# Optimization experiments

Hardware: AMD Instinct MI355X
Metric: run time of the kernel (lower is better)

## Reference

```python
import jax, jax.numpy as jnp
import numpy as np
from jax import lax

EPS = 1e-05
DN = ('NHWC', 'HWIO', 'NHWC')


def setup_inputs() -> dict:
    key = jax.random.key(0)
    k1, k2, k3 = jax.random.split(key, 3)
    x = jax.random.normal(k1, (16, 64, 64, 128), dtype=jnp.float32)
    kernel = jax.random.normal(k2, (3, 3, 128, 256), dtype=jnp.float32) * 0.05
    bias = jax.random.normal(k3, (256,), dtype=jnp.float32) * 0.01
    alpha = jnp.ones((1,), dtype=jnp.float32)
    return {"x": x, "kernel": kernel, "bias": bias, "alpha": alpha}


def reference(x, kernel, bias, alpha):
    # dot-product conv: <patch, W> per output channel  -> [B,H,W,O]
    dot = lax.conv_general_dilated(x, kernel, (1, 1), 'SAME', dimension_numbers=DN)
    # per-patch squared norm ||x_patch||^2 via conv of x^2 with ones kernel -> [B,H,W,1]
    ones_k = jnp.ones(kernel.shape[:-1] + (1,), dtype=x.dtype)
    patch_sq = lax.conv_general_dilated(x * x, ones_k, (1, 1), 'SAME', dimension_numbers=DN)
    # per-output-channel squared kernel norm ||W_o||^2 -> [O]
    kernel_sq = jnp.sum(kernel * kernel, axis=(0, 1, 2))
    # ||x - W||^2 = ||x||^2 - 2<x,W> + ||W||^2
    dist_sq = patch_sq - 2.0 * dot + kernel_sq
    y = (dot * dot) / (dist_sq + EPS)
    y = y + bias
    out_features = kernel.shape[-1]
    scale = (jnp.sqrt(jnp.float32(out_features)) / jnp.log1p(jnp.float32(out_features))) ** alpha
    return y * scale
```

## Files before the change

### kernel.cpp

```cpp
#include <hip/hip_runtime.h>
#include <stdint.h>


#define HH 64
#define WW 64
#define CC 128
#define OO 256
#define HP 66
#define WP 66
#define NPIX (16 * HP * WP)
#define KTOT 1152
#define NKT 18
#define EPSV 1e-5f

#define BM 256
#define BN 128
#define SLOT_BYTES 49152
#define B_OFF 32768
#define SMEM_TOTAL (3 * SLOT_BYTES + 1024)

typedef short short8 __attribute__((ext_vector_type(8)));
typedef float f32x4 __attribute__((ext_vector_type(4)));

__device__ __forceinline__ unsigned short f2bf(float f) {
  unsigned u = __builtin_bit_cast(unsigned, f);
  u += 0x7fffu + ((u >> 16) & 1u);
  return (unsigned short)(u >> 16);
}

__device__ __forceinline__ void gload_lds16(const void* g, void* l) {
  __builtin_amdgcn_global_load_lds(
      (const __attribute__((address_space(1))) unsigned int*)g,
      (__attribute__((address_space(3))) unsigned int*)l,
      16, 0, 0);
}

#define FENCE() asm volatile("" ::: "memory")
#define BAR() do { FENCE(); __builtin_amdgcn_s_barrier(); FENCE(); } while (0)

__global__ __launch_bounds__(256) void prep_x(const float* __restrict__ x,
                                              unsigned short* __restrict__ xp,
                                              float* __restrict__ s2p) {
  int lane = threadIdx.x & 63;
  int wv = (blockIdx.x << 2) + (threadIdx.x >> 6);
  for (int gw = wv; gw < NPIX; gw += 4096) {
    int b = gw / (HP * WP);
    int rem = gw - b * (HP * WP);
    int hp = rem / WP;
    int wp = rem - hp * WP;
    float2 v = make_float2(0.f, 0.f);
    if (hp >= 1 && hp <= HH && wp >= 1 && wp <= WW) {
      const float2* src = (const float2*)(x + (size_t)(((b * HH) + hp - 1) * WW + (wp - 1)) * CC);
      v = src[lane];
    }
    ushort2 o2;
    o2.x = f2bf(v.x);
    o2.y = f2bf(v.y);
    ((ushort2*)(xp + (size_t)gw * CC))[lane] = o2;
    float ss = v.x * v.x + v.y * v.y;
    #pragma unroll
    for (int off = 32; off > 0; off >>= 1) ss += __shfl_down(ss, off);
    if (lane == 0) s2p[gw] = ss;
  }
}

__global__ __launch_bounds__(256) void prep_w(const float* __restrict__ kern,
                                              unsigned short* __restrict__ wt,
                                              float* __restrict__ ksq) {
  int o = blockIdx.x;
  int t = threadIdx.x;
  float acc = 0.f;
  for (int k = t; k < KTOT; k += 256) {
    float v = kern[(size_t)k * OO + o];
    wt[(size_t)o * KTOT + k] = f2bf(v);
    acc += v * v;
  }
  __shared__ float red[256];
  red[t] = acc;
  __syncthreads();
  #pragma unroll
  for (int s = 128; s > 0; s >>= 1) {
    if (t < s) red[t] += red[t + s];
    __syncthreads();
  }
  if (t == 0) ksq[o] = red[0];
}

__global__ __launch_bounds__(512, 2) void yat_main(
    const unsigned short* __restrict__ xp,
    const unsigned short* __restrict__ wt,
    const float* __restrict__ s2p,
    const float* __restrict__ ksq,
    const float* __restrict__ bias,
    const float* __restrict__ alpha,
    float* __restrict__ out) {
  extern __shared__ char smem[];

  int tid = threadIdx.x;
  int wid = tid >> 6, lane = tid & 63;

  int bid = blockIdx.x;
  int swz = ((bid & 7) << 6) + (bid >> 3);
  int mt = swz >> 1, nt = swz & 1;
  int m0 = mt << 8;
  int n0 = nt << 7;

  int cg = (((tid & 7) ^ ((tid >> 3) & 7)) << 3);
  const unsigned short* aSrc[4];
  #pragma unroll
  for (int q = 0; q < 4; ++q) {
    int r = (q << 6) + (tid >> 3);
    int p = m0 + r;
    int b = p >> 12, h = (p >> 6) & 63, w = p & 63;
    aSrc[q] = xp + (size_t)((b * HP + h) * WP + w) * CC + cg;
  }
  const unsigned short* bSrc[2];
  #pragma unroll
  for (int q = 0; q < 2; ++q) {
    int r = (q << 6) + (tid >> 3);
    bSrc[q] = wt + (size_t)(n0 + r) * KTOT + cg;
  }

  auto STAGE = [&](int t, int soff) {
    int tap = t >> 1;
    int dy = tap / 3;
    int dx = tap - dy * 3;
    int koff = (dy * WP + dx) * CC + ((t & 1) << 6);
    char* da = smem + soff + (wid << 10);
    #pragma unroll
    for (int q = 0; q < 4; ++q)
      gload_lds16(aSrc[q] + koff, da + (q << 13));
    int kb = t << 6;
    char* db = smem + soff + B_OFF + (wid << 10);
    #pragma unroll
    for (int q = 0; q < 2; ++q)
      gload_lds16(bSrc[q] + kb, db + (q << 13));
  };

  int wr = wid >> 1, wcn = wid & 1;
  int rA0 = (wr << 6) + (lane & 15);
  int rB0 = (wcn << 6) + (lane & 15);
  int xsw = lane & 7;
  int co0 = (((lane >> 4) ^ xsw) << 4);
  int co1 = ((((lane >> 4) + 4) ^ xsw) << 4);

  f32x4 acc[4][4] = {};

  STAGE(0, 0);
  STAGE(1, SLOT_BYTES);

  int soff = 0;
  int stoff = 2 * SLOT_BYTES;
  for (int i = 0; i < NKT; ++i) {
    if (i < NKT - 2) STAGE(i + 2, stoff);
    if (i < NKT - 2)      asm volatile("s_waitcnt vmcnt(12)" ::: "memory");
    else if (i == NKT - 2) asm volatile("s_waitcnt vmcnt(6)" ::: "memory");
    else                   asm volatile("s_waitcnt vmcnt(0)" ::: "memory");
    BAR();

    const char* Ab = smem + soff;
    const char* Bb = Ab + B_OFF;
    short8 af[2][4], bf[2][4];
    #pragma unroll
    for (int ks = 0; ks < 2; ++ks) {
      int co = ks ? co1 : co0;
      #pragma unroll
      for (int m = 0; m < 4; ++m)
        af[ks][m] = *(const short8*)(Ab + ((rA0 + (m << 4)) << 7) + co);
      #pragma unroll
      for (int n = 0; n < 4; ++n)
        bf[ks][n] = *(const short8*)(Bb + ((rB0 + (n << 4)) << 7) + co);
    }
    __builtin_amdgcn_s_setprio(1);
    #pragma unroll
    for (int ks = 0; ks < 2; ++ks) {
      #pragma unroll
      for (int m = 0; m < 4; ++m) {
        #pragma unroll
        for (int n = 0; n < 4; ++n)
          acc[m][n] = __builtin_amdgcn_mfma_f32_16x16x32_bf16(af[ks][m], bf[ks][n], acc[m][n], 0, 0, 0);
      }
    }
    __builtin_amdgcn_s_setprio(0);
    asm volatile("s_waitcnt lgkmcnt(0)" ::: "memory");
    BAR();

    soff += SLOT_BYTES;  if (soff == 3 * SLOT_BYTES) soff = 0;
    stoff += SLOT_BYTES; if (stoff == 3 * SLOT_BYTES) stoff = 0;
  }

  float* ps = (float*)(smem + 3 * SLOT_BYTES);
  if (tid < BM) {
    int p = m0 + tid;
    int b = p >> 12, h = (p >> 6) & 63, w = p & 63;
    const float* s2 = s2p + (b * HP + h) * WP + w;
    float s = 0.f;
    #pragma unroll
    for (int dy = 0; dy < 3; ++dy) {
      #pragma unroll
      for (int dx = 0; dx < 3; ++dx) s += s2[dy * WP + dx];
    }
    ps[tid] = s;
  }
  asm volatile("s_waitcnt lgkmcnt(0)" ::: "memory");
  BAR();

  float al = alpha[0];
  float scale = powf(16.0f / logf(257.0f), al);

  int c0 = n0 + (wcn << 6) + (lane & 15);
  int rb = (wr << 6) + ((lane >> 4) << 2);
  #pragma unroll
  for (int n = 0; n < 4; ++n) {
    int cn = c0 + (n << 4);
    float kq = ksq[cn] + EPSV;
    float bv = bias[cn];
    #pragma unroll
    for (int m = 0; m < 4; ++m) {
      f32x4 a = acc[m][n];
      #pragma unroll
      for (int j = 0; j < 4; ++j) {
        int rm = rb + (m << 4) + j;
        float dot = a[j];
        float dist = ps[rm] - 2.0f * dot + kq;
        float y = dot * dot / dist + bv;
        out[(size_t)(m0 + rm) * OO + cn] = y * scale;
      }
    }
  }
}

extern "C" void kernel_launch(void* const* d_in, const int* in_sizes, int n_in,
                              void* d_out, int out_size, void* d_ws, size_t ws_size,
                              hipStream_t stream) {
  const float* x = (const float*)d_in[0];
  const float* kern = (const float*)d_in[1];
  const float* bias = (const float*)d_in[2];
  const float* alpha = (const float*)d_in[3];
  float* out = (float*)d_out;

  char* ws = (char*)d_ws;
  unsigned short* xp  = (unsigned short*)ws;
  unsigned short* wtb = (unsigned short*)(ws + 17842176);
  float* s2p = (float*)(ws + 18432000);
  float* ksq = (float*)(ws + 18710784);

  (void)hipFuncSetAttribute((const void*)yat_main,
                            hipFuncAttributeMaxDynamicSharedMemorySize, SMEM_TOTAL);

  prep_x<<<1024, 256, 0, stream>>>(x, xp, s2p);
  prep_w<<<256, 256, 0, stream>>>(kern, wtb, ksq);
  yat_main<<<512, 512, SMEM_TOTAL, stream>>>(xp, wtb, s2p, ksq, bias, alpha, out);
}
```

Before: 156.8 us.

## Enlarge GEMM tile to 256x256 with BK=32 four-stage split A/B pipeline

Result: faster. 150.9 us (-3.8%).

```diff
diff --git a/kernel.cpp b/kernel.cpp
--- a/kernel.cpp
+++ b/kernel.cpp
@@ -10,14 +10,15 @@
 #define WP 66
 #define NPIX (16 * HP * WP)
 #define KTOT 1152
-#define NKT 18
+#define BK 32
+#define NKT 36
 #define EPSV 1e-5f
 
-#define BM 256
-#define BN 128
-#define SLOT_BYTES 49152
-#define B_OFF 32768
-#define SMEM_TOTAL (3 * SLOT_BYTES + 1024)
+#define SLOT 16384
+#define A_BASE 0
+#define B_BASE 65536
+#define PS_OFF 131072
+#define SMEM_TOTAL (131072 + 1024)
 
 typedef short short8 __attribute__((ext_vector_type(8)));
 typedef float f32x4 __attribute__((ext_vector_type(4)));
@@ -100,97 +101,101 @@
   int wid = tid >> 6, lane = tid & 63;
 
   int bid = blockIdx.x;
-  int swz = ((bid & 7) << 6) + (bid >> 3);
-  int mt = swz >> 1, nt = swz & 1;
+  int mt = ((bid & 7) << 5) + (bid >> 3);
   int m0 = mt << 8;
-  int n0 = nt << 7;
-
-  int cg = (((tid & 7) ^ ((tid >> 3) & 7)) << 3);
-  const unsigned short* aSrc[4];
-  #pragma unroll
-  for (int q = 0; q < 4; ++q) {
-    int r = (q << 6) + (tid >> 3);
-    int p = m0 + r;
+
+  int g = ((lane & 3) ^ ((lane >> 3) & 3)) << 3;
+  const unsigned short* aS[2];
+  #pragma unroll
+  for (int d = 0; d < 2; ++d) {
+    int p = m0 + (wid << 5) + (d << 4) + (lane >> 2);
     int b = p >> 12, h = (p >> 6) & 63, w = p & 63;
-    aSrc[q] = xp + (size_t)((b * HP + h) * WP + w) * CC + cg;
-  }
-  const unsigned short* bSrc[2];
-  #pragma unroll
-  for (int q = 0; q < 2; ++q) {
-    int r = (q << 6) + (tid >> 3);
-    bSrc[q] = wt + (size_t)(n0 + r) * KTOT + cg;
-  }
-
-  auto STAGE = [&](int t, int soff) {
-    int tap = t >> 1;
-    int dy = tap / 3;
-    int dx = tap - dy * 3;
-    int koff = (dy * WP + dx) * CC + ((t & 1) << 6);
-    char* da = smem + soff + (wid << 10);
-    #pragma unroll
-    for (int q = 0; q < 4; ++q)
-      gload_lds16(aSrc[q] + koff, da + (q << 13));
-    int kb = t << 6;
-    char* db = smem + soff + B_OFF + (wid << 10);
-    #pragma unroll
-    for (int q = 0; q < 2; ++q)
-      gload_lds16(bSrc[q] + kb, db + (q << 13));
+    aS[d] = xp + (size_t)((b * HP + h) * WP + w) * CC + g;
+  }
+  const unsigned short* bS[2];
+  #pragma unroll
+  for (int d = 0; d < 2; ++d) {
+    int o = (wid << 5) + (d << 4) + (lane >> 2);
+    bS[d] = wt + (size_t)o * KTOT + g;
+  }
+
+  auto STAGE_A = [&](int t) {
+    int tap = t >> 2, q = t & 3;
+    int dy = tap / 3, dx = tap - dy * 3;
+    int koff = (dy * WP + dx) * CC + (q << 5);
+    char* dst = smem + A_BASE + ((t & 3) << 14) + (wid << 11);
+    gload_lds16(aS[0] + koff, dst);
+    gload_lds16(aS[1] + koff, dst + 1024);
   };
-
-  int wr = wid >> 1, wcn = wid & 1;
-  int rA0 = (wr << 6) + (lane & 15);
-  int rB0 = (wcn << 6) + (lane & 15);
-  int xsw = lane & 7;
-  int co0 = (((lane >> 4) ^ xsw) << 4);
-  int co1 = ((((lane >> 4) + 4) ^ xsw) << 4);
-
-  f32x4 acc[4][4] = {};
-
-  STAGE(0, 0);
-  STAGE(1, SLOT_BYTES);
-
-  int soff = 0;
-  int stoff = 2 * SLOT_BYTES;
-  for (int i = 0; i < NKT; ++i) {
-    if (i < NKT - 2) STAGE(i + 2, stoff);
-    if (i < NKT - 2)      asm volatile("s_waitcnt vmcnt(12)" ::: "memory");
-    else if (i == NKT - 2) asm volatile("s_waitcnt vmcnt(6)" ::: "memory");
+  auto STAGE_B = [&](int t) {
+    int koff = t << 5;
+    char* dst = smem + B_BASE + ((t & 3) << 14) + (wid << 11);
+    gload_lds16(bS[0] + koff, dst);
+    gload_lds16(bS[1] + koff, dst + 1024);
+  };
+
+  int wr = wid >> 2, wc = wid & 3;
+  int csw = (((lane >> 4) ^ ((lane >> 1) & 3)) << 4);
+  int aOff[8], bOff[4];
+  #pragma unroll
+  for (int m = 0; m < 8; ++m)
+    aOff[m] = (((wr << 7) + (m << 4) + (lane & 15)) << 6) + csw;
+  #pragma unroll
+  for (int n = 0; n < 4; ++n)
+    bOff[n] = (((wc << 6) + (n << 4) + (lane & 15)) << 6) + csw;
+
+  f32x4 acc[8][4] = {};
+
+  STAGE_A(0); STAGE_B(0);
+  STAGE_A(1); STAGE_B(1);
+  STAGE_A(2); STAGE_B(2);
+  asm volatile("s_waitcnt vmcnt(8)" ::: "memory");
+  BAR();
+
+  #pragma unroll 1
+  for (int t = 0; t < NKT; ++t) {
+    const char* sA = smem + A_BASE + ((t & 3) << 14);
+    const char* sB = smem + B_BASE + ((t & 3) << 14);
+    short8 af[8], bf[4];
+
+    #pragma unroll
+    for (int m = 0; m < 4; ++m) af[m] = *(const short8*)(sA + aOff[m]);
+    #pragma unroll
+    for (int n = 0; n < 4; ++n) bf[n] = *(const short8*)(sB + bOff[n]);
+    BAR();
+    if (t + 3 < NKT) STAGE_A(t + 3);
+    asm volatile("s_waitcnt lgkmcnt(0)" ::: "memory");
+    __builtin_amdgcn_sched_barrier(0);
+    __builtin_amdgcn_s_setprio(1);
+    #pragma unroll
+    for (int m = 0; m < 4; ++m) {
+      #pragma unroll
+      for (int n = 0; n < 4; ++n)
+        acc[m][n] = __builtin_amdgcn_mfma_f32_16x16x32_bf16(af[m], bf[n], acc[m][n], 0, 0, 0);
+    }
+    __builtin_amdgcn_s_setprio(0);
+
+    #pragma unroll
+    for (int m = 4; m < 8; ++m) af[m] = *(const short8*)(sA + aOff[m]);
+    if (t < NKT - 3)       asm volatile("s_waitcnt vmcnt(6)" ::: "memory");
+    else if (t == NKT - 3) asm volatile("s_waitcnt vmcnt(4)" ::: "memory");
     else                   asm volatile("s_waitcnt vmcnt(0)" ::: "memory");
     BAR();
-
-    const char* Ab = smem + soff;
-    const char* Bb = Ab + B_OFF;
-    short8 af[2][4], bf[2][4];
-    #pragma unroll
-    for (int ks = 0; ks < 2; ++ks) {
-      int co = ks ? co1 : co0;
-      #pragma unroll
-      for (int m = 0; m < 4; ++m)
-        af[ks][m] = *(const short8*)(Ab + ((rA0 + (m << 4)) << 7) + co);
+    if (t + 3 < NKT) STAGE_B(t + 3);
+    asm volatile("s_waitcnt lgkmcnt(0)" ::: "memory");
+    __builtin_amdgcn_sched_barrier(0);
+    __builtin_amdgcn_s_setprio(1);
+    #pragma unroll
+    for (int m = 4; m < 8; ++m) {
       #pragma unroll
       for (int n = 0; n < 4; ++n)
-        bf[ks][n] = *(const short8*)(Bb + ((rB0 + (n << 4)) << 7) + co);
-    }
-    __builtin_amdgcn_s_setprio(1);
-    #pragma unroll
-    for (int ks = 0; ks < 2; ++ks) {
-      #pragma unroll
-      for (int m = 0; m < 4; ++m) {
-        #pragma unroll
-        for (int n = 0; n < 4; ++n)
-          acc[m][n] = __builtin_amdgcn_mfma_f32_16x16x32_bf16(af[ks][m], bf[ks][n], acc[m][n], 0, 0, 0);
-      }
+        acc[m][n] = __builtin_amdgcn_mfma_f32_16x16x32_bf16(af[m], bf[n], acc[m][n], 0, 0, 0);
     }
     __builtin_amdgcn_s_setprio(0);
-    asm volatile("s_waitcnt lgkmcnt(0)" ::: "memory");
-    BAR();
-
-    soff += SLOT_BYTES;  if (soff == 3 * SLOT_BYTES) soff = 0;
-    stoff += SLOT_BYTES; if (stoff == 3 * SLOT_BYTES) stoff = 0;
-  }
-
-  float* ps = (float*)(smem + 3 * SLOT_BYTES);
-  if (tid < BM) {
+  }
+
+  float* ps = (float*)(smem + PS_OFF);
+  if (tid < 256) {
     int p = m0 + tid;
     int b = p >> 12, h = (p >> 6) & 63, w = p & 63;
     const float* s2 = s2p + (b * HP + h) * WP + w;
@@ -208,15 +213,15 @@
   float al = alpha[0];
   float scale = powf(16.0f / logf(257.0f), al);
 
-  int c0 = n0 + (wcn << 6) + (lane & 15);
-  int rb = (wr << 6) + ((lane >> 4) << 2);
+  int c0 = (wc << 6) + (lane & 15);
+  int rb = (wr << 7) + ((lane >> 4) << 2);
   #pragma unroll
   for (int n = 0; n < 4; ++n) {
     int cn = c0 + (n << 4);
     float kq = ksq[cn] + EPSV;
     float bv = bias[cn];
     #pragma unroll
-    for (int m = 0; m < 4; ++m) {
+    for (int m = 0; m < 8; ++m) {
       f32x4 a = acc[m][n];
       #pragma unroll
       for (int j = 0; j < 4; ++j) {
@@ -250,5 +255,5 @@
 
   prep_x<<<1024, 256, 0, stream>>>(x, xp, s2p);
   prep_w<<<256, 256, 0, stream>>>(kern, wtb, ksq);
-  yat_main<<<512, 512, SMEM_TOTAL, stream>>>(xp, wtb, s2p, ksq, bias, alpha, out);
-}
+  yat_main<<<256, 512, SMEM_TOTAL, stream>>>(xp, wtb, s2p, ksq, bias, alpha, out);
+}
```
